# Kernel optimization log

Measured on AMD Instinct MI355X. Metric: run time of the kernel, lower is better.

Reference implementation:

```python
import jax, jax.numpy as jnp
import numpy as np

B, Ng, C, H, W, Nt, M, P = 4, 8192, 256, 128, 128, 512, 8, 4
Ch = C // M  # 32 channels per head
EPS = 1e-5


def setup_inputs():
    key = jax.random.key(0)
    ks = jax.random.split(key, 12)
    s = 0.02
    def w(k, shape):
        return jax.random.normal(k, shape, jnp.float32) * s
    return {
        "query": jax.random.normal(ks[0], (B, Ng, C), jnp.float32),
        "value": jax.random.normal(ks[1], (B, C, H, W), jnp.float32),
        "reference_points": jax.random.uniform(ks[2], (B, Ng, 2), dtype=jnp.float32),
        "trajectory_points": jax.random.uniform(ks[3], (B, Nt, 2), dtype=jnp.float32),
        "in_proj_w": w(ks[4], (3 * C, C)),
        "in_proj_b": jnp.zeros((3 * C,), jnp.float32),
        "mha_out_w": w(ks[5], (C, C)),
        "mha_out_b": jnp.zeros((C,), jnp.float32),
        "ln_g": jnp.ones((C,), jnp.float32),
        "ln_b": jnp.zeros((C,), jnp.float32),
        "traj_w": w(ks[6], (C, 2)),
        "traj_b": jnp.zeros((C,), jnp.float32),
        "offs_w": w(ks[7], (M * P * 2, C)),
        "offs_b": jnp.zeros((M * P * 2,), jnp.float32),
        "attw_w": w(ks[8], (M * P, C)),
        "attw_b": jnp.zeros((M * P,), jnp.float32),
        "out_w": w(ks[9], (C, C)),
        "out_b": jnp.zeros((C,), jnp.float32),
    }


def _bilinear_sample(imgf, x, y):
    # imgf: (NM, Ch, H*W); x, y: (NM, Lq, P) unnormalized pixel coords
    # grid_sample semantics: bilinear, padding_mode='zeros', align_corners=False
    NM = imgf.shape[0]
    Lq, Pp = x.shape[1], x.shape[2]
    x0 = jnp.floor(x); y0 = jnp.floor(y)
    x1 = x0 + 1.0;     y1 = y0 + 1.0

    def gather(xi, yi):
        valid = (xi >= 0) & (xi < W) & (yi >= 0) & (yi < H)
        xc = jnp.clip(xi, 0, W - 1).astype(jnp.int32)
        yc = jnp.clip(yi, 0, H - 1).astype(jnp.int32)
        idx = (yc * W + xc).reshape(NM, 1, Lq * Pp)
        v = jnp.take_along_axis(imgf, jnp.broadcast_to(idx, (NM, Ch, Lq * Pp)), axis=2)
        return v.reshape(NM, Ch, Lq, Pp), valid.astype(imgf.dtype)

    v00, m00 = gather(x0, y0)
    v01, m01 = gather(x1, y0)
    v10, m10 = gather(x0, y1)
    v11, m11 = gather(x1, y1)
    wx1 = x - x0; wx0 = 1.0 - wx1
    wy1 = y - y0; wy0 = 1.0 - wy1
    out = (v00 * (wx0 * wy0 * m00)[:, None]
         + v01 * (wx1 * wy0 * m01)[:, None]
         + v10 * (wx0 * wy1 * m10)[:, None]
         + v11 * (wx1 * wy1 * m11)[:, None])
    return out  # (NM, Ch, Lq, P)


def reference(query, value, reference_points, trajectory_points,
              in_proj_w, in_proj_b, mha_out_w, mha_out_b, ln_g, ln_b,
              traj_w, traj_b, offs_w, offs_b, attw_w, attw_b, out_w, out_b):
    # trajectory projection: (B,Nt,2) -> (B,Nt,C)
    tf = trajectory_points @ traj_w.T + traj_b

    # guidance cross-attention (nn.MultiheadAttention, eval mode => no dropout)
    wq, wk, wv = jnp.split(in_proj_w, 3, axis=0)
    bq, bk, bv = jnp.split(in_proj_b, 3, axis=0)
    q = (query @ wq.T + bq).reshape(B, Ng, M, Ch)
    k = (tf @ wk.T + bk).reshape(B, Nt, M, Ch)
    v = (tf @ wv.T + bv).reshape(B, Nt, M, Ch)
    scores = jnp.einsum('bqmc,bkmc->bmqk', q, k) / jnp.sqrt(jnp.float32(Ch))
    probs = jax.nn.softmax(scores, axis=-1)
    ctx = jnp.einsum('bmqk,bkmc->bqmc', probs, v).reshape(B, Ng, C)
    ctx = ctx @ mha_out_w.T + mha_out_b

    # residual + LayerNorm
    x = query + ctx
    mu = x.mean(-1, keepdims=True)
    var = ((x - mu) ** 2).mean(-1, keepdims=True)
    gq = (x - mu) / jnp.sqrt(var + EPS) * ln_g + ln_b

    # sampling offsets & softmax attention weights (L=1 level)
    offs = (gq @ offs_w.T + offs_b).reshape(B, Ng, M, 1, P, 2)
    aw = jax.nn.softmax((gq @ attw_w.T + attw_b).reshape(B, Ng, M, P), axis=-1)
    loc = reference_points[:, :, None, None, None, :] + offs  # (B,Ng,M,1,P,2)

    # deformable sampling core (single level)
    grid = 2.0 * loc[:, :, :, 0] - 1.0                   # (B,Ng,M,P,2)
    grid = grid.transpose(0, 2, 1, 3, 4).reshape(B * M, Ng, P, 2)
    gx = (grid[..., 0] + 1.0) * (W * 0.5) - 0.5
    gy = (grid[..., 1] + 1.0) * (H * 0.5) - 0.5
    imgf = value.reshape(B * M, Ch, H * W)               # per-head feature maps
    samp = _bilinear_sample(imgf, gx, gy)                # (B*M,Ch,Ng,P)
    w_att = aw.transpose(0, 2, 1, 3).reshape(B * M, 1, Ng, P)
    out = (samp * w_att).sum(-1)                         # (B*M,Ch,Ng)

    # faithful to source: view(B,M,Ch,Ng).transpose(1,2).contiguous().view(B,Ng,C)
    out = out.reshape(B, M, Ch, Ng).transpose(0, 2, 1, 3).reshape(B, Ng, C)
    return out @ out_w.T + out_b
```

## Files before the change

kernel.cpp:

```cpp
#include <hip/hip_runtime.h>
#include <hip/hip_bf16.h>
#include <stdint.h>

typedef __bf16 bf16_t;
typedef __bf16 bf16x8 __attribute__((ext_vector_type(8)));
typedef __bf16 bf16x4 __attribute__((ext_vector_type(4)));
typedef float f32x4 __attribute__((ext_vector_type(4)));

#define CEXP 0.25506807186679906f

__device__ __forceinline__ float ldf(const void* p, size_t i, int isf) {
  return isf ? ((const float*)p)[i] : (float)((const bf16_t*)p)[i];
}

__device__ __forceinline__ int detect_isf(const void* q) {
  const uint16_t* u = (const uint16_t*)q;
  const int lane = threadIdx.x & 63;
  const uint16_t v = u[2 * lane];
  const int e = (v >> 7) & 0xFF;
  const int weird = (e >= 0x86 || (v != 0 && e <= 0x65)) ? 1 : 0;
  return (__popcll(__ballot(weird)) >= 16) ? 1 : 0;
}

__device__ __forceinline__ float fexp2(float x) {
#if __has_builtin(__builtin_amdgcn_exp2f)
  return __builtin_amdgcn_exp2f(x);
#else
  return exp2f(x);
#endif
}

__device__ __forceinline__ f32x4 mfma16x16x16(bf16x4 a, bf16x4 b, f32x4 c) {
#if __has_builtin(__builtin_amdgcn_mfma_f32_16x16x16_bf16)
  return __builtin_amdgcn_mfma_f32_16x16x16_bf16(a, b, c, 0, 0, 0);
#else
  typedef short s16x4 __attribute__((ext_vector_type(4)));
  return __builtin_amdgcn_mfma_f32_16x16x16bf16_1k(
      __builtin_bit_cast(s16x4, a), __builtin_bit_cast(s16x4, b), c, 0, 0, 0);
#endif
}

__device__ __forceinline__ void stage16(const bf16_t* g, bf16_t* l) {
  __builtin_amdgcn_global_load_lds((const __attribute__((address_space(1))) void*)g,
                                   (__attribute__((address_space(3))) void*)l, 16, 0, 0);
}

__global__ __launch_bounds__(256) void prep_all(
    const void* __restrict__ query,
    const void* in_w, const void* in_b, const void* mow, const void* mob,
    const void* outw, const void* outb,
    const void* trajp, const void* tw, const void* tb,
    const void* offs_w, const void* attw_w, const void* offs_b, const void* attw_b,
    bf16_t* __restrict__ blob, bf16_t* __restrict__ tf,
    bf16_t* __restrict__ Wph, bf16_t* __restrict__ Wpl, bf16_t* __restrict__ bp)
{
  const int isf = detect_isf(query);
  const int bid = blockIdx.x;
  if (bid < 322) {
    const int g = (bid * 256 + threadIdx.x) * 4;
    if (g >= 328960) return;
    const void* src; size_t off;
    if      (g < 196608) { src = in_w; off = g; }
    else if (g < 197376) { src = in_b; off = g - 196608; }
    else if (g < 262912) { src = mow;  off = g - 197376; }
    else if (g < 263168) { src = mob;  off = g - 262912; }
    else if (g < 328704) { src = outw; off = g - 263168; }
    else                 { src = outb; off = g - 328704; }
#pragma unroll
    for (int k = 0; k < 4; k++) blob[g + k] = (bf16_t)ldf(src, off + k, isf);
  } else if (bid < 322 + 2048) {
    const int rowb = bid - 322;
    const int c = threadIdx.x;
    const float x = ldf(trajp, rowb * 2 + 0, isf);
    const float y = ldf(trajp, rowb * 2 + 1, isf);
    const float v = x * ldf(tw, c * 2 + 0, isf) + y * ldf(tw, c * 2 + 1, isf) + ldf(tb, c, isf);
    tf[(size_t)rowb * 256 + c] = (bf16_t)v;
  } else {
    const int idx = (bid - 2370) * 256 + threadIdx.x;
    const int rowp = idx >> 8, c = idx & 255;
    float v = 0.0f;
    if (rowp < 64)      v = ldf(offs_w, rowp * 256 + c, isf);
    else if (rowp < 96) v = ldf(attw_w, (rowp - 64) * 256 + c, isf);
    const bf16_t hi = (bf16_t)v;
    Wph[idx] = hi;
    Wpl[idx] = (bf16_t)(v - (float)hi);
    if (idx < 128) {
      float bv = 0.0f;
      if (idx < 64)      bv = ldf(offs_b, idx, isf);
      else if (idx < 96) bv = ldf(attw_b, idx - 64, isf);
      bp[idx] = (bf16_t)bv;
    }
  }
}

#define TM 128
#define TN 128
#define TKK 64

__global__ __launch_bounds__(256) void gemm_async(
    const bf16_t* __restrict__ A, const bf16_t* __restrict__ W,
    const bf16_t* __restrict__ bias, void* __restrict__ Cout,
    void* __restrict__ Cout2, int Ndim, int Kdim, int mode, float kscale,
    const void* __restrict__ qdet)
{
  __shared__ __align__(16) bf16_t As[TM * TKK];
  __shared__ __align__(16) bf16_t Ws[TN * TKK];
  const int t    = threadIdx.x;
  const int lane = t & 63;
  const int w    = t >> 6;
  const int wm   = (w & 1) * 64;
  const int wn   = (w >> 1) * 64;
  const int q4   = lane >> 4;
  const int r16  = lane & 15;
  const int tm   = blockIdx.x * TM;
  const int tn   = blockIdx.y * TN;

  f32x4 acc[4][4] = {};

  for (int kt = 0; kt < Kdim; kt += TKK) {
    __syncthreads();
#pragma unroll
    for (int r = 0; r < 4; r++) {
      const int L = w * 256 + r * 64 + lane;
      const int R = L >> 3, c = (L & 7) * 8;
      stage16(A + (size_t)(tm + R) * Kdim + kt + c, As + L * 8);
      stage16(W + (size_t)(tn + R) * Kdim + kt + c, Ws + L * 8);
    }
    __syncthreads();
#pragma unroll
    for (int ks = 0; ks < TKK; ks += 32) {
      bf16x8 af[4], bfm[4];
#pragma unroll
      for (int i = 0; i < 4; i++)
        af[i] = *(const bf16x8*)(As + (wm + 16 * i + r16) * TKK + ks + q4 * 8);
#pragma unroll
      for (int j = 0; j < 4; j++)
        bfm[j] = *(const bf16x8*)(Ws + (wn + 16 * j + r16) * TKK + ks + q4 * 8);
#pragma unroll
      for (int i = 0; i < 4; i++)
#pragma unroll
        for (int j = 0; j < 4; j++)
          acc[i][j] = __builtin_amdgcn_mfma_f32_16x16x32_bf16(af[i], bfm[j], acc[i][j], 0, 0, 0);
    }
  }

  const int isf = (mode == 3) ? detect_isf(qdet) : 1;
#pragma unroll
  for (int j = 0; j < 4; j++) {
    const int col = tn + wn + 16 * j + r16;
    const float bv = (float)bias[col];
#pragma unroll
    for (int i = 0; i < 4; i++) {
      const int row0 = tm + wm + 16 * i + q4 * 4;
#pragma unroll
      for (int rr = 0; rr < 4; rr++) {
        const float v = acc[i][j][rr] + bv;
        const size_t off = (size_t)(row0 + rr) * Ndim + col;
        if (mode == 0) {
          ((bf16_t*)Cout)[off] = (bf16_t)v;
        } else if (mode == 6) {
          const int rowg = row0 + rr;
          if (col < 256) {
            ((bf16_t*)Cout)[(size_t)rowg * 256 + col] = (bf16_t)(v * kscale);
          } else {
            const int bb = rowg >> 9, tt = rowg & 511;
            const int c2 = col - 256;
            const int mm = c2 >> 5, ch = c2 & 31;
            ((bf16_t*)Cout2)[(((size_t)(bb * 8 + mm) * 32 + ch) << 9) + tt] = (bf16_t)v;
          }
        } else {
          if (isf) ((float*)Cout)[off] = v; else ((bf16_t*)Cout)[off] = (bf16_t)v;
        }
      }
    }
  }
}

__global__ __launch_bounds__(256) void gemm_f32a(
    const void* __restrict__ Araw, const bf16_t* __restrict__ W,
    const bf16_t* __restrict__ bias, bf16_t* __restrict__ Cout,
    int Ndim, int Kdim, const void* __restrict__ qdet)
{
  __shared__ __align__(16) bf16_t As[TM * TKK];
  __shared__ __align__(16) bf16_t Ws[TN * TKK];
  const int t    = threadIdx.x;
  const int lane = t & 63;
  const int w    = t >> 6;
  const int wm   = (w & 1) * 64;
  const int wn   = (w >> 1) * 64;
  const int q4   = lane >> 4;
  const int r16  = lane & 15;
  const int tm   = blockIdx.x * TM;
  const int tn   = blockIdx.y * TN;
  const int aisf = detect_isf(qdet);

  f32x4 acc[4][4] = {};
  const int srow = t >> 1;
  const int skb  = (t & 1) * 32;

  for (int kt = 0; kt < Kdim; kt += TKK) {
    __syncthreads();
    if (aisf) {
      const float4* ga = (const float4*)((const float*)Araw + (size_t)(tm + srow) * Kdim + kt + skb);
#pragma unroll
      for (int kk = 0; kk < 8; kk++) {
        const float4 u = ga[kk];
        bf16x4 h = {(bf16_t)u.x, (bf16_t)u.y, (bf16_t)u.z, (bf16_t)u.w};
        *(bf16x4*)(As + srow * TKK + skb + kk * 4) = h;
      }
    } else {
      const uint4* ga = (const uint4*)((const bf16_t*)Araw + (size_t)(tm + srow) * Kdim + kt + skb);
      uint4* la = (uint4*)(As + srow * TKK + skb);
      la[0] = ga[0]; la[1] = ga[1]; la[2] = ga[2]; la[3] = ga[3];
    }
    {
      const uint4* gw = (const uint4*)(W + (size_t)(tn + srow) * Kdim + kt + skb);
      uint4* lw = (uint4*)(Ws + srow * TKK + skb);
      lw[0] = gw[0]; lw[1] = gw[1]; lw[2] = gw[2]; lw[3] = gw[3];
    }
    __syncthreads();
#pragma unroll
    for (int ks = 0; ks < TKK; ks += 32) {
      bf16x8 af[4], bfm[4];
#pragma unroll
      for (int i = 0; i < 4; i++)
        af[i] = *(const bf16x8*)(As + (wm + 16 * i + r16) * TKK + ks + q4 * 8);
#pragma unroll
      for (int j = 0; j < 4; j++)
        bfm[j] = *(const bf16x8*)(Ws + (wn + 16 * j + r16) * TKK + ks + q4 * 8);
#pragma unroll
      for (int i = 0; i < 4; i++)
#pragma unroll
        for (int j = 0; j < 4; j++)
          acc[i][j] = __builtin_amdgcn_mfma_f32_16x16x32_bf16(af[i], bfm[j], acc[i][j], 0, 0, 0);
    }
  }

#pragma unroll
  for (int j = 0; j < 4; j++) {
    const int col = tn + wn + 16 * j + r16;
    const float bv = (float)bias[col];
#pragma unroll
    for (int i = 0; i < 4; i++) {
      const int row0 = tm + wm + 16 * i + q4 * 4;
#pragma unroll
      for (int rr = 0; rr < 4; rr++)
        Cout[(size_t)(row0 + rr) * Ndim + col] = (bf16_t)(acc[i][j][rr] + bv);
    }
  }
}

__global__ __launch_bounds__(256, 2) void attn_kernel(
    const bf16_t* __restrict__ Q, const bf16_t* __restrict__ Kk,
    const bf16_t* __restrict__ Vt, bf16_t* __restrict__ ctx)
{
  const int t = threadIdx.x;
  const int lane = t & 63, w = t >> 6;
  const int q4 = lane >> 4, r16 = lane & 15;
  const int bm = blockIdx.y;
  const int b = bm >> 3, m = bm & 7;
  const int q0 = blockIdx.x * 512 + w * 128;

  bf16x8 qf[8];
#pragma unroll
  for (int qt = 0; qt < 8; qt++)
    qf[qt] = *(const bf16x8*)(Q + ((size_t)(b * 8192 + q0 + qt * 16 + r16) * 256 + m * 32 + q4 * 8));

  f32x4 acc[8][2] = {};
  float lsum[8] = {0.f, 0.f, 0.f, 0.f, 0.f, 0.f, 0.f, 0.f};

  const bf16_t* kbase  = Kk + (size_t)b * 512 * 256 + m * 32 + (size_t)r16 * 256 + q4 * 8;
  const bf16_t* vbase0 = Vt + (size_t)bm * 32 * 512 + ((size_t)r16 << 9) + q4 * 4;
  const bf16_t* vbase1 = vbase0 + (16 << 9);

  bf16x8 kfA = *(const bf16x8*)(kbase);
  bf16x4 v0A = *(const bf16x4*)(vbase0);
  bf16x4 v1A = *(const bf16x4*)(vbase1);
  bf16x8 kfB = *(const bf16x8*)(kbase + (size_t)16 * 256);
  bf16x4 v0B = *(const bf16x4*)(vbase0 + 16);
  bf16x4 v1B = *(const bf16x4*)(vbase1 + 16);

  for (int k0 = 0; k0 < 512; k0 += 32) {
    const bf16x8 ka = kfA;
    const bf16x4 va0 = v0A, va1 = v1A;
    kfA = *(const bf16x8*)(kbase + (size_t)(k0 + 32) * 256);
    v0A = *(const bf16x4*)(vbase0 + k0 + 32);
    v1A = *(const bf16x4*)(vbase1 + k0 + 32);
    __builtin_amdgcn_s_setprio(1);
#pragma unroll
    for (int qt = 0; qt < 8; qt++) {
      f32x4 z = {};
      const f32x4 s = __builtin_amdgcn_mfma_f32_16x16x32_bf16(ka, qf[qt], z, 0, 0, 0);
      const float e0 = fexp2(s[0]), e1 = fexp2(s[1]);
      const float e2 = fexp2(s[2]), e3 = fexp2(s[3]);
      lsum[qt] += (e0 + e1) + (e2 + e3);
      const bf16x4 p = {(bf16_t)e0, (bf16_t)e1, (bf16_t)e2, (bf16_t)e3};
      acc[qt][0] = mfma16x16x16(va0, p, acc[qt][0]);
      acc[qt][1] = mfma16x16x16(va1, p, acc[qt][1]);
    }
    __builtin_amdgcn_s_setprio(0);
    const bf16x8 kb = kfB;
    const bf16x4 vb0 = v0B, vb1 = v1B;
    kfB = *(const bf16x8*)(kbase + (size_t)(k0 + 48) * 256);
    v0B = *(const bf16x4*)(vbase0 + k0 + 48);
    v1B = *(const bf16x4*)(vbase1 + k0 + 48);
    __builtin_amdgcn_s_setprio(1);
#pragma unroll
    for (int qt = 0; qt < 8; qt++) {
      f32x4 z = {};
      const f32x4 s = __builtin_amdgcn_mfma_f32_16x16x32_bf16(kb, qf[qt], z, 0, 0, 0);
      const float e0 = fexp2(s[0]), e1 = fexp2(s[1]);
      const float e2 = fexp2(s[2]), e3 = fexp2(s[3]);
      lsum[qt] += (e0 + e1) + (e2 + e3);
      const bf16x4 p = {(bf16_t)e0, (bf16_t)e1, (bf16_t)e2, (bf16_t)e3};
      acc[qt][0] = mfma16x16x16(vb0, p, acc[qt][0]);
      acc[qt][1] = mfma16x16x16(vb1, p, acc[qt][1]);
    }
    __builtin_amdgcn_s_setprio(0);
  }

#pragma unroll
  for (int qt = 0; qt < 8; qt++) {
    float v = lsum[qt];
    v += __shfl_xor(v, 16, 64);
    v += __shfl_xor(v, 32, 64);
    const float inv = 1.0f / v;
    const size_t row = (size_t)b * 8192 + q0 + qt * 16 + r16;
    bf16x4 o0, o1;
#pragma unroll
    for (int rr = 0; rr < 4; rr++) {
      o0[rr] = (bf16_t)(acc[qt][0][rr] * inv);
      o1[rr] = (bf16_t)(acc[qt][1][rr] * inv);
    }
    *(bf16x4*)(ctx + row * 256 + m * 32 + q4 * 4)      = o0;
    *(bf16x4*)(ctx + row * 256 + m * 32 + 16 + q4 * 4) = o1;
  }
}

__global__ __launch_bounds__(256) void ln_kernel(
    const bf16_t* __restrict__ y2, const void* __restrict__ query,
    const void* __restrict__ g, const void* __restrict__ beta,
    bf16_t* __restrict__ gqh, bf16_t* __restrict__ gql)
{
  const int isf = detect_isf(query);
  const int rowb = blockIdx.x * 4 + (threadIdx.x >> 6);
  const int lane = threadIdx.x & 63;
  const size_t base = (size_t)rowb * 256;
  const int c0 = lane * 4;
  float x[4];
  {
    const bf16x4 yv = *(const bf16x4*)(y2 + base + c0);
    if (isf) {
      const float4 qv = *(const float4*)((const float*)query + base + c0);
      x[0] = qv.x + (float)yv[0]; x[1] = qv.y + (float)yv[1];
      x[2] = qv.z + (float)yv[2]; x[3] = qv.w + (float)yv[3];
    } else {
      const bf16x4 qv = *(const bf16x4*)((const bf16_t*)query + base + c0);
#pragma unroll
      for (int k = 0; k < 4; k++) x[k] = (float)qv[k] + (float)yv[k];
    }
  }
  float s = x[0] + x[1] + x[2] + x[3];
  for (int d = 1; d < 64; d <<= 1) s += __shfl_xor(s, d, 64);
  const float mu = s * (1.0f / 256.0f);
  float vs = 0.f;
#pragma unroll
  for (int k = 0; k < 4; k++) { const float d = x[k] - mu; vs += d * d; }
  for (int d = 1; d < 64; d <<= 1) vs += __shfl_xor(vs, d, 64);
  const float rstd = rsqrtf(vs * (1.0f / 256.0f) + 1e-5f);
  float gw[4], bb[4];
  if (isf) {
    const float4 gg = *(const float4*)((const float*)g + c0);
    const float4 bv = *(const float4*)((const float*)beta + c0);
    gw[0] = gg.x; gw[1] = gg.y; gw[2] = gg.z; gw[3] = gg.w;
    bb[0] = bv.x; bb[1] = bv.y; bb[2] = bv.z; bb[3] = bv.w;
  } else {
    const bf16x4 gg = *(const bf16x4*)((const bf16_t*)g + c0);
    const bf16x4 bv = *(const bf16x4*)((const bf16_t*)beta + c0);
#pragma unroll
    for (int k = 0; k < 4; k++) { gw[k] = (float)gg[k]; bb[k] = (float)bv[k]; }
  }
  bf16x4 hi4, lo4;
#pragma unroll
  for (int k = 0; k < 4; k++) {
    const float gv = (x[k] - mu) * rstd * gw[k] + bb[k];
    const bf16_t hi = (bf16_t)gv;
    hi4[k] = hi;
    lo4[k] = (bf16_t)(gv - (float)hi);
  }
  *(bf16x4*)(gqh + base + c0) = hi4;
  *(bf16x4*)(gql + base + c0) = lo4;
}

__global__ __launch_bounds__(256) void gemm_offs(
    const bf16_t* __restrict__ Ahg, const bf16_t* __restrict__ Alg,
    const bf16_t* __restrict__ Whg, const bf16_t* __restrict__ Wlg,
    const bf16_t* __restrict__ bias, float* __restrict__ Cout)
{
  __shared__ __align__(16) bf16_t Ah[128 * 64];
  __shared__ __align__(16) bf16_t Al[128 * 64];
  __shared__ __align__(16) bf16_t Wh[128 * 64];
  __shared__ __align__(16) bf16_t Wl[128 * 64];
  const int t    = threadIdx.x;
  const int lane = t & 63;
  const int w    = t >> 6;
  const int wm   = (w & 1) * 64;
  const int wn   = (w >> 1) * 64;
  const int q4   = lane >> 4;
  const int r16  = lane & 15;
  const int tm   = blockIdx.x * 128;

  f32x4 acc[4][4] = {};
  const int srow = t >> 1;
  const int skb  = (t & 1) * 32;

  for (int kt = 0; kt < 256; kt += 64) {
    __syncthreads();
    {
      const uint4* g0 = (const uint4*)(Ahg + (size_t)(tm + srow) * 256 + kt + skb);
      uint4* l0 = (uint4*)(Ah + srow * 64 + skb);
      l0[0] = g0[0]; l0[1] = g0[1]; l0[2] = g0[2]; l0[3] = g0[3];
      const uint4* g1 = (const uint4*)(Alg + (size_t)(tm + srow) * 256 + kt + skb);
      uint4* l1 = (uint4*)(Al + srow * 64 + skb);
      l1[0] = g1[0]; l1[1] = g1[1]; l1[2] = g1[2]; l1[3] = g1[3];
      const uint4* g2 = (const uint4*)(Whg + (size_t)srow * 256 + kt + skb);
      uint4* l2 = (uint4*)(Wh + srow * 64 + skb);
      l2[0] = g2[0]; l2[1] = g2[1]; l2[2] = g2[2]; l2[3] = g2[3];
      const uint4* g3 = (const uint4*)(Wlg + (size_t)srow * 256 + kt + skb);
      uint4* l3 = (uint4*)(Wl + srow * 64 + skb);
      l3[0] = g3[0]; l3[1] = g3[1]; l3[2] = g3[2]; l3[3] = g3[3];
    }
    __syncthreads();
#pragma unroll
    for (int ks = 0; ks < 64; ks += 32) {
      bf16x8 ah[4], al[4], bh[4], bl[4];
#pragma unroll
      for (int i = 0; i < 4; i++) {
        ah[i] = *(const bf16x8*)(Ah + (wm + 16 * i + r16) * 64 + ks + q4 * 8);
        al[i] = *(const bf16x8*)(Al + (wm + 16 * i + r16) * 64 + ks + q4 * 8);
      }
#pragma unroll
      for (int j = 0; j < 4; j++) {
        bh[j] = *(const bf16x8*)(Wh + (wn + 16 * j + r16) * 64 + ks + q4 * 8);
        bl[j] = *(const bf16x8*)(Wl + (wn + 16 * j + r16) * 64 + ks + q4 * 8);
      }
#pragma unroll
      for (int i = 0; i < 4; i++)
#pragma unroll
        for (int j = 0; j < 4; j++) {
          f32x4 a = acc[i][j];
          a = __builtin_amdgcn_mfma_f32_16x16x32_bf16(al[i], bh[j], a, 0, 0, 0);
          a = __builtin_amdgcn_mfma_f32_16x16x32_bf16(ah[i], bl[j], a, 0, 0, 0);
          a = __builtin_amdgcn_mfma_f32_16x16x32_bf16(ah[i], bh[j], a, 0, 0, 0);
          acc[i][j] = a;
        }
    }
  }

#pragma unroll
  for (int j = 0; j < 4; j++) {
    const int col = wn + 16 * j + r16;
    const float bv = (float)bias[col];
#pragma unroll
    for (int i = 0; i < 4; i++) {
      const int row0 = tm + wm + 16 * i + q4 * 4;
#pragma unroll
      for (int rr = 0; rr < 4; rr++)
        Cout[(size_t)(row0 + rr) * 128 + col] = acc[i][j][rr] + bv;
    }
  }
}

__global__ __launch_bounds__(256) void transpose_value(
    const void* __restrict__ V, bf16_t* __restrict__ Vp, const void* __restrict__ qdet)
{
  __shared__ __align__(16) bf16_t tile[32][136];
  const int isf = detect_isf(qdet);
  const int bid = blockIdx.x;
  const int h = bid & 127;
  const int bm = bid >> 7;
  const int b = bm >> 3, mm = bm & 7;
  const int t = threadIdx.x;
  const int ch  = t >> 3;
  const int ww0 = (t & 7) * 16;
  const size_t ibase = (((size_t)b * 256 + mm * 32 + ch) * 128 + h) * 128 + ww0;
  if (isf) {
    const float4* src = (const float4*)((const float*)V + ibase);
    bf16x8 h0, h1;
#pragma unroll
    for (int k = 0; k < 2; k++) {
      const float4 u0 = src[k * 2], u1 = src[k * 2 + 1];
      bf16x8 hh = {(bf16_t)u0.x, (bf16_t)u0.y, (bf16_t)u0.z, (bf16_t)u0.w,
                   (bf16_t)u1.x, (bf16_t)u1.y, (bf16_t)u1.z, (bf16_t)u1.w};
      if (k == 0) h0 = hh; else h1 = hh;
    }
    *(bf16x8*)(&tile[ch][ww0])     = h0;
    *(bf16x8*)(&tile[ch][ww0 + 8]) = h1;
  } else {
    const bf16x8* src = (const bf16x8*)((const bf16_t*)V + ibase);
    *(bf16x8*)(&tile[ch][ww0])     = src[0];
    *(bf16x8*)(&tile[ch][ww0 + 8]) = src[1];
  }
  __syncthreads();
  const size_t base = ((size_t)bm * 128 + h) * 4096;
  const int ww = t >> 1;
  const int c0 = (t & 1) * 16;
  bf16x8 o0, o1;
#pragma unroll
  for (int e = 0; e < 8; e++) { o0[e] = tile[c0 + e][ww]; o1[e] = tile[c0 + 8 + e][ww]; }
  *(bf16x8*)(Vp + base + ww * 32 + c0)     = o0;
  *(bf16x8*)(Vp + base + ww * 32 + c0 + 8) = o1;
}

__global__ __launch_bounds__(256) void sampler(
    const float* __restrict__ ys, const void* __restrict__ refp,
    const bf16_t* __restrict__ vperm, bf16_t* __restrict__ outs,
    const void* __restrict__ qdet)
{
  const int isf = detect_isf(qdet);
  const int t = threadIdx.x;
  const int wg = blockIdx.x;
  const int bm = (wg & 7) + ((wg >> 8) << 3);
  const int qt = (wg >> 3) & 31;
  const int b = bm >> 3, m = bm & 7;
  const int qq = qt * 256 + t;
  const size_t row = (size_t)b * 8192 + qq;
  const float* y = ys + row * 128;
  const float rx = ldf(refp, row * 2 + 0, isf);
  const float ry = ldf(refp, row * 2 + 1, isf);

  const float l0 = y[64 + m * 4 + 0], l1 = y[64 + m * 4 + 1];
  const float l2 = y[64 + m * 4 + 2], l3 = y[64 + m * 4 + 3];
  const float mx = fmaxf(fmaxf(l0, l1), fmaxf(l2, l3));
  const float e0 = __expf(l0 - mx), e1 = __expf(l1 - mx);
  const float e2 = __expf(l2 - mx), e3 = __expf(l3 - mx);
  const float inv = 1.0f / (e0 + e1 + e2 + e3);
  const float aw[4] = {e0 * inv, e1 * inv, e2 * inv, e3 * inv};

  float acc[32];
#pragma unroll
  for (int ch = 0; ch < 32; ch++) acc[ch] = 0.0f;

  const bf16_t* vbase = vperm + (size_t)bm * (128 * 128 * 32);

  for (int p = 0; p < 4; p++) {
    const float gx = (rx + y[m * 8 + p * 2 + 0]) * 128.0f - 0.5f;
    const float gy = (ry + y[m * 8 + p * 2 + 1]) * 128.0f - 0.5f;
    const float x0f = floorf(gx), y0f = floorf(gy);
    const int x0 = (int)x0f, y0i = (int)y0f;
    const float wx1 = gx - x0f, wx0 = 1.0f - wx1;
    const float wy1 = gy - y0f, wy0 = 1.0f - wy1;
    const float a = aw[p];
    for (int cy = 0; cy < 2; cy++) {
      const int yy = y0i + cy;
      if (yy < 0 || yy >= 128) continue;
      const float wy = cy ? wy1 : wy0;
      for (int cx = 0; cx < 2; cx++) {
        const int xx = x0 + cx;
        if (xx < 0 || xx >= 128) continue;
        const float wgt = a * wy * (cx ? wx1 : wx0);
        const bf16x8* src8 = (const bf16x8*)(vbase + ((size_t)yy * 128 + xx) * 32);
#pragma unroll
        for (int vv = 0; vv < 4; vv++) {
          const bf16x8 d = src8[vv];
#pragma unroll
          for (int e = 0; e < 8; e++) acc[vv * 8 + e] += wgt * (float)d[e];
        }
      }
    }
  }

  const size_t obase = (size_t)b * 8192;
#pragma unroll
  for (int ch = 0; ch < 32; ch++) {
    const size_t orow = obase + (size_t)(ch * 8 + m) * 32 + qt;
    outs[orow * 256 + t] = (bf16_t)acc[ch];
  }
}

extern "C" void kernel_launch(void* const* d_in, const int* in_sizes, int n_in,
                              void* d_out, int out_size, void* d_ws, size_t ws_size,
                              hipStream_t stream) {
  const void* query = d_in[0];
  const void* value = d_in[1];
  const void* refp  = d_in[2];
  const void* trajp = d_in[3];
  const void* in_w  = d_in[4];
  const void* in_b  = d_in[5];
  const void* mow   = d_in[6];
  const void* mob   = d_in[7];
  const void* lng   = d_in[8];
  const void* lnb   = d_in[9];
  const void* tw    = d_in[10];
  const void* tb    = d_in[11];
  const void* ow    = d_in[12];
  const void* ob    = d_in[13];
  const void* aww   = d_in[14];
  const void* awb   = d_in[15];
  const void* outw  = d_in[16];
  const void* outb  = d_in[17];

  char* base = (char*)d_ws;
  float*  ysamp = (float*)(base);
  bf16_t* qout  = (bf16_t*)(base + 16777216);
  bf16_t* ctx   = (bf16_t*)(base + 33554432);
  bf16_t* y2    = (bf16_t*)(base + 50331648);
  bf16_t* tf_ws = (bf16_t*)(base + 67108864);
  bf16_t* k_ws  = (bf16_t*)(base + 68157440);
  bf16_t* vt_g  = (bf16_t*)(base + 69206016);
  bf16_t* blob  = (bf16_t*)(base + 70254592);

  bf16_t* gqh   = qout;
  bf16_t* gql   = ctx;
  bf16_t* vperm = (bf16_t*)(base + 16777216);
  bf16_t* outs  = y2;

  bf16_t* inw_bf  = blob;
  bf16_t* inb_bf  = blob + 196608;
  bf16_t* mow_bf  = blob + 197376;
  bf16_t* mob_bf  = blob + 262912;
  bf16_t* outw_bf = blob + 263168;
  bf16_t* outb_bf = blob + 328704;
  bf16_t* wph     = blob + 328960;
  bf16_t* wpl     = blob + 361728;
  bf16_t* bpad    = blob + 394496;

  prep_all<<<dim3(2498), dim3(256), 0, stream>>>(
      query, in_w, in_b, mow, mob, outw, outb, trajp, tw, tb,
      ow, aww, ob, awb, blob, tf_ws, wph, wpl, bpad);
  gemm_async<<<dim3(16, 4), dim3(256), 0, stream>>>(
      tf_ws, inw_bf + 65536, inb_bf + 256, (void*)k_ws, (void*)vt_g, 512, 256, 6, CEXP, query);
  gemm_f32a<<<dim3(256, 2), dim3(256), 0, stream>>>(
      query, inw_bf, inb_bf, qout, 256, 256, query);
  attn_kernel<<<dim3(16, 32), dim3(256), 0, stream>>>(qout, k_ws, vt_g, ctx);
  gemm_async<<<dim3(256, 2), dim3(256), 0, stream>>>(
      ctx, mow_bf, mob_bf, (void*)y2, nullptr, 256, 256, 0, 1.0f, query);
  ln_kernel<<<dim3(8192), dim3(256), 0, stream>>>(y2, query, lng, lnb, gqh, gql);
  gemm_offs<<<dim3(256, 1), dim3(256), 0, stream>>>(gqh, gql, wph, wpl, bpad, ysamp);
  transpose_value<<<dim3(4096), dim3(256), 0, stream>>>(value, vperm, query);
  sampler<<<dim3(1024), dim3(256), 0, stream>>>(ysamp, refp, vperm, outs, query);
  gemm_async<<<dim3(256, 2), dim3(256), 0, stream>>>(
      outs, outw_bf, outb_bf, d_out, nullptr, 256, 256, 3, 1.0f, query);
}
```

Before: 347.8 us.

## Store offsets per head contiguously and split sampler channels across two blocks

The offsets GEMM epilogue now writes its 96 live columns into a per-(batch,head) layout of 16 floats per query, and drops the padded columns. This lets the sampler fetch its offsets and logits with three float4 loads instead of scattered strided reads. The sampler grid doubles, with each block handling 16 of the 32 channels. That halves per-thread accumulators and raises parallelism, but the index math and softmax are now computed twice.

```diff
diff --git a/kernel.cpp b/kernel.cpp
--- a/kernel.cpp
+++ b/kernel.cpp
@@ -461,12 +461,20 @@
   for (int j = 0; j < 4; j++) {
     const int col = wn + 16 * j + r16;
     const float bv = (float)bias[col];
+    const int live  = (col < 96) ? 1 : 0;
+    const int moff  = (col < 64) ? (col >> 3) : ((col - 64) >> 2);
+    const int inner = (col < 64) ? (col & 7) : (8 + (col & 3));
 #pragma unroll
     for (int i = 0; i < 4; i++) {
       const int row0 = tm + wm + 16 * i + q4 * 4;
 #pragma unroll
-      for (int rr = 0; rr < 4; rr++)
-        Cout[(size_t)(row0 + rr) * 128 + col] = acc[i][j][rr] + bv;
+      for (int rr = 0; rr < 4; rr++) {
+        if (live) {
+          const int row = row0 + rr;
+          const int bq = row >> 13, q = row & 8191;
+          Cout[(((size_t)(bq * 8 + moff) << 13) + q) * 16 + inner] = acc[i][j][rr] + bv;
+        }
+      }
     }
   }
 }
@@ -513,39 +521,45 @@
 }
 
 __global__ __launch_bounds__(256) void sampler(
-    const float* __restrict__ ys, const void* __restrict__ refp,
+    const float* __restrict__ ys2, const void* __restrict__ refp,
     const bf16_t* __restrict__ vperm, bf16_t* __restrict__ outs,
     const void* __restrict__ qdet)
 {
   const int isf = detect_isf(qdet);
   const int t = threadIdx.x;
   const int wg = blockIdx.x;
-  const int bm = (wg & 7) + ((wg >> 8) << 3);
-  const int qt = (wg >> 3) & 31;
+  const int bm  = (wg & 7) + ((wg >> 9) << 3);
+  const int mid = (wg >> 3) & 63;
+  const int qt  = mid >> 1;
+  const int hf  = mid & 1;
   const int b = bm >> 3, m = bm & 7;
   const int qq = qt * 256 + t;
   const size_t row = (size_t)b * 8192 + qq;
-  const float* y = ys + row * 128;
+  const float* y16 = ys2 + (((size_t)bm << 13) + qq) * 16;
   const float rx = ldf(refp, row * 2 + 0, isf);
   const float ry = ldf(refp, row * 2 + 1, isf);
 
-  const float l0 = y[64 + m * 4 + 0], l1 = y[64 + m * 4 + 1];
-  const float l2 = y[64 + m * 4 + 2], l3 = y[64 + m * 4 + 3];
-  const float mx = fmaxf(fmaxf(l0, l1), fmaxf(l2, l3));
-  const float e0 = __expf(l0 - mx), e1 = __expf(l1 - mx);
-  const float e2 = __expf(l2 - mx), e3 = __expf(l3 - mx);
+  const float4 off01 = *(const float4*)(y16 + 0);
+  const float4 off23 = *(const float4*)(y16 + 4);
+  const float4 lg    = *(const float4*)(y16 + 8);
+
+  const float mx = fmaxf(fmaxf(lg.x, lg.y), fmaxf(lg.z, lg.w));
+  const float e0 = __expf(lg.x - mx), e1 = __expf(lg.y - mx);
+  const float e2 = __expf(lg.z - mx), e3 = __expf(lg.w - mx);
   const float inv = 1.0f / (e0 + e1 + e2 + e3);
   const float aw[4] = {e0 * inv, e1 * inv, e2 * inv, e3 * inv};
-
-  float acc[32];
-#pragma unroll
-  for (int ch = 0; ch < 32; ch++) acc[ch] = 0.0f;
-
-  const bf16_t* vbase = vperm + (size_t)bm * (128 * 128 * 32);
+  const float ox[4] = {off01.x, off01.z, off23.x, off23.z};
+  const float oy[4] = {off01.y, off01.w, off23.y, off23.w};
+
+  float acc[16];
+#pragma unroll
+  for (int ch = 0; ch < 16; ch++) acc[ch] = 0.0f;
+
+  const bf16_t* vbase = vperm + (size_t)bm * (128 * 128 * 32) + hf * 16;
 
   for (int p = 0; p < 4; p++) {
-    const float gx = (rx + y[m * 8 + p * 2 + 0]) * 128.0f - 0.5f;
-    const float gy = (ry + y[m * 8 + p * 2 + 1]) * 128.0f - 0.5f;
+    const float gx = (rx + ox[p]) * 128.0f - 0.5f;
+    const float gy = (ry + oy[p]) * 128.0f - 0.5f;
     const float x0f = floorf(gx), y0f = floorf(gy);
     const int x0 = (int)x0f, y0i = (int)y0f;
     const float wx1 = gx - x0f, wx0 = 1.0f - wx1;
@@ -560,11 +574,12 @@
         if (xx < 0 || xx >= 128) continue;
         const float wgt = a * wy * (cx ? wx1 : wx0);
         const bf16x8* src8 = (const bf16x8*)(vbase + ((size_t)yy * 128 + xx) * 32);
-#pragma unroll
-        for (int vv = 0; vv < 4; vv++) {
-          const bf16x8 d = src8[vv];
-#pragma unroll
-          for (int e = 0; e < 8; e++) acc[vv * 8 + e] += wgt * (float)d[e];
+        const bf16x8 d0 = src8[0];
+        const bf16x8 d1 = src8[1];
+#pragma unroll
+        for (int e = 0; e < 8; e++) {
+          acc[e]     += wgt * (float)d0[e];
+          acc[8 + e] += wgt * (float)d1[e];
         }
       }
     }
@@ -572,8 +587,9 @@
 
   const size_t obase = (size_t)b * 8192;
 #pragma unroll
-  for (int ch = 0; ch < 32; ch++) {
-    const size_t orow = obase + (size_t)(ch * 8 + m) * 32 + qt;
+  for (int ch = 0; ch < 16; ch++) {
+    const int chg = hf * 16 + ch;
+    const size_t orow = obase + (size_t)(chg * 8 + m) * 32 + qt;
     outs[orow * 256 + t] = (bf16_t)acc[ch];
   }
 }
@@ -638,7 +654,7 @@
   ln_kernel<<<dim3(8192), dim3(256), 0, stream>>>(y2, query, lng, lnb, gqh, gql);
   gemm_offs<<<dim3(256, 1), dim3(256), 0, stream>>>(gqh, gql, wph, wpl, bpad, ysamp);
   transpose_value<<<dim3(4096), dim3(256), 0, stream>>>(value, vperm, query);
-  sampler<<<dim3(1024), dim3(256), 0, stream>>>(ysamp, refp, vperm, outs, query);
+  sampler<<<dim3(2048), dim3(256), 0, stream>>>(ysamp, refp, vperm, outs, query);
   gemm_async<<<dim3(256, 2), dim3(256), 0, stream>>>(
       outs, outw_bf, outb_bf, d_out, nullptr, 256, 256, 3, 1.0f, query);
 }
```

New measurement: 336.3 us. -3.3%, faster.
